# Kernel tuning notes

Measured on AMD Instinct MI355X. Metric: run time of the kernel, lower is better.

Reference implementation:

```python
import jax, jax.numpy as jnp
import numpy as np

G = 128          # resolution
NE = 4           # n_emotions
SIGMA = 0.05     # splat kernel width
ETA = 0.01       # global write strength
ALPHA_H = 0.002
ALPHA_E = 0.001
LEAK = 5e-05
RADIUS = max(2, int(3.0 * SIGMA * G / 2.0))   # = 9
W = 2 * RADIUS + 1                            # = 19


def _laplacian(x):
    # 6-neighbor Laplacian with replicate padding; x: [..., G, G, G]
    pad = [(0, 0)] * (x.ndim - 3) + [(1, 1)] * 3
    p = jnp.pad(x, pad, mode='edge')
    c = p[..., 1:-1, 1:-1, 1:-1]
    return (p[..., :-2, 1:-1, 1:-1] + p[..., 2:, 1:-1, 1:-1]
            + p[..., 1:-1, :-2, 1:-1] + p[..., 1:-1, 2:, 1:-1]
            + p[..., 1:-1, 1:-1, :-2] + p[..., 1:-1, 1:-1, 2:]
            - 6.0 * c)


def _splat(H, E, positions, intensities, emotions):
    # Gaussian splat scatter-add into H [G,G,G] and E [NE,G,G,G].
    gp = (positions + 1.0) * 0.5 * (G - 1)                       # [N,3] grid coords
    c = jnp.clip(jnp.floor(gp).astype(jnp.int32), 0, G - 1)      # center cell
    offs = jnp.arange(-RADIUS, RADIUS + 1, dtype=jnp.int32)
    coords = c[:, :, None] + offs[None, None, :]                 # [N,3,W]
    valid = (coords >= 0) & (coords < G)
    cc = jnp.clip(coords, 0, G - 1)
    sig = SIGMA * G / 2.0
    d = coords.astype(gp.dtype) - gp[:, :, None]                 # [N,3,W]
    k1 = jnp.where(valid, jnp.exp(-(d * d) / (2.0 * sig * sig)), 0.0)
    kx, ky, kz = k1[:, 0], k1[:, 1], k1[:, 2]                    # [N,W] each (separable)
    omega = intensities * ETA                                    # [N]
    vals = (omega[:, None, None, None] * kx[:, :, None, None]
            * ky[:, None, :, None] * kz[:, None, None, :])       # [N,W,W,W]
    flat = ((cc[:, 0][:, :, None, None] * G + cc[:, 1][:, None, :, None]) * G
            + cc[:, 2][:, None, None, :]).reshape(-1)            # [N*W^3]
    H_new = H.reshape(-1).at[flat].add(vals.reshape(-1)).reshape(G, G, G)
    E_ch = []
    for e in range(NE):
        ve = (vals * emotions[:, e][:, None, None, None]).reshape(-1)
        E_ch.append(E[e].reshape(-1).at[flat].add(ve).reshape(G, G, G))
    return H_new, jnp.stack(E_ch)


def _step(H, E):
    H2 = jnp.maximum(H * (1.0 - LEAK) + ALPHA_H * _laplacian(H), 0.0)
    E2 = jnp.maximum(E * (1.0 - LEAK) + LEAK + ALPHA_E * _laplacian(E), 0.0)
    return H2, E2


def _sample(H, E, sp):
    # grid_sample trilinear, padding_mode='border', align_corners=True.
    # grid_sample axis convention: sp[...,0]->last axis, sp[...,1]->middle, sp[...,2]->first.
    B, T, _ = sp.shape
    t = jnp.clip((sp.reshape(-1, 3) + 1.0) * 0.5 * (G - 1), 0.0, G - 1)  # [BT,3]
    i0 = jnp.floor(t).astype(jnp.int32)
    f = t - i0
    i0 = jnp.clip(i0, 0, G - 1)
    i1 = jnp.clip(i0 + 1, 0, G - 1)
    x0, y0, z0 = i0[:, 0], i0[:, 1], i0[:, 2]
    x1, y1, z1 = i1[:, 0], i1[:, 1], i1[:, 2]
    fx, fy, fz = f[:, 0], f[:, 1], f[:, 2]

    def interp(vol):  # vol [..., G,G,G] -> [..., BT]
        out = 0.0
        for zi, wz in ((z0, 1.0 - fz), (z1, fz)):
            for yi, wy in ((y0, 1.0 - fy), (y1, fy)):
                for xi, wx in ((x0, 1.0 - fx), (x1, fx)):
                    out = out + vol[..., zi, yi, xi] * (wz * wy * wx)
        return out

    p_H = interp(H).reshape(B, T)
    p_E = interp(E).T.reshape(B, T, NE)
    return p_H, p_E


def setup_inputs() -> dict:
    key = jax.random.key(0)
    k1, k2, k3, k4 = jax.random.split(key, 4)
    N, B, T = 4096, 8, 1024
    return {
        'positions': jax.random.uniform(k1, (N, 3), jnp.float32, -0.95, 0.95),
        'intensities': jax.random.uniform(k2, (N,), jnp.float32),
        'emotions': jax.random.uniform(k3, (N, NE), jnp.float32),
        'sample_positions': jax.random.uniform(k4, (B, T, 3), jnp.float32, -1.0, 1.0),
        'H0': jnp.zeros((G, G, G), jnp.float32),
        'E0': jnp.ones((NE, G, G, G), jnp.float32),
    }


def reference(positions, intensities, emotions, sample_positions, H0, E0):
    H, E = _splat(H0, E0, positions, intensities, emotions)
    H, E = _step(H, E)
    p_H, p_E = _sample(H, E, sample_positions)
    return jnp.concatenate([p_H[..., None], p_E], axis=-1)  # [B,T,1+NE]
```

## Files before the change

### kernel.cpp

```cpp
#include <hip/hip_runtime.h>


namespace {
constexpr int   G      = 128;
constexpr int   G3     = G * G * G;
constexpr int   NE     = 4;
constexpr int   RAD    = 9;
constexpr float SIG    = 0.05f * (float)G * 0.5f;
constexpr float INV2S2 = 1.0f / (2.0f * SIG * SIG);
constexpr float ETA    = 0.01f;
constexpr float A_H    = 0.002f;
constexpr float A_E    = 0.001f;
constexpr float LEAK   = 5e-5f;

constexpr int T0 = 4, T1 = 4, T2 = 32;
constexpr int NT0 = G / T0, NT1 = G / T1, NT2 = G / T2;
constexpr int NTILES = NT0 * NT1 * NT2;
constexpr int CAP = 96;
}

__device__ __forceinline__ int clampi(int v, int lo, int hi) {
    return min(max(v, lo), hi);
}

__global__ void __launch_bounds__(256) bin_meta_kernel(
        const float* __restrict__ pos, const float* __restrict__ inten,
        const float4* __restrict__ emo4,
        int* __restrict__ counts, int* __restrict__ lists,
        float4* __restrict__ meta, int N) {
    const int p    = blockIdx.x * 4 + (threadIdx.x >> 6);
    const int lane = threadIdx.x & 63;
    if (p >= N) return;

    const float gx = (pos[p * 3 + 0] + 1.0f) * 0.5f * (float)(G - 1);
    const float gy = (pos[p * 3 + 1] + 1.0f) * 0.5f * (float)(G - 1);
    const float gz = (pos[p * 3 + 2] + 1.0f) * 0.5f * (float)(G - 1);
    const int c0 = clampi((int)floorf(gx), 0, G - 1);
    const int c1 = clampi((int)floorf(gy), 0, G - 1);
    const int c2 = clampi((int)floorf(gz), 0, G - 1);

    if (lane == 0) {
        meta[2 * p]     = make_float4(gx, gy, gz, inten[p] * ETA);
        meta[2 * p + 1] = emo4[p];
    }

    const int l0 = max(c0 - RAD, 0) >> 2, h0 = min(c0 + RAD, G - 1) >> 2;
    const int l1 = max(c1 - RAD, 0) >> 2, h1 = min(c1 + RAD, G - 1) >> 2;
    const int l2 = max(c2 - RAD, 0) >> 5, h2 = min(c2 + RAD, G - 1) >> 5;
    const int n0 = h0 - l0, n1 = h1 - l1, n2 = h2 - l2;

    for (int s = lane; s < 72; s += 64) {
        const int a = s / 12;
        const int r = s - a * 12;
        const int b = r >> 1;
        const int cs = r & 1;
        if (a <= n0 && b <= n1 && cs <= n2) {
            const int t = ((l0 + a) * NT1 + (l1 + b)) * NT2 + (l2 + cs);
            const int slot = atomicAdd(&counts[t], 1);
            if (slot < CAP) lists[t * CAP + slot] = p;
        }
    }
}

__global__ void __launch_bounds__(256) gather_kernel(
        const float4* __restrict__ meta,
        const float* __restrict__ H0, const float* __restrict__ E0,
        const int* __restrict__ counts, const int* __restrict__ lists,
        float* __restrict__ ws) {
    const int tile = blockIdx.x;
    const int t2 = tile % NT2, t1 = (tile / NT2) % NT1, t0 = tile / (NT2 * NT1);
    const int tid = threadIdx.x;

    __shared__ float kx[CAP * 4];
    __shared__ float ky[CAP * 4];
    __shared__ float kz[CAP * 32];

    const int cnt = min(counts[tile], CAP);
    const int* __restrict__ lst = lists + tile * CAP;

    const int b0 = t0 * T0, b1 = t1 * T1, b2 = t2 * T2;
    for (int t = tid; t < cnt * 40; t += 256) {
        const int n = t / 40;
        const int s = t - n * 40;
        const int p = lst[n];
        const int axis = (s < 4) ? 0 : (s < 8) ? 1 : 2;
        const int off  = (s < 4) ? s : (s < 8) ? s - 4 : s - 8;
        const float4 mg = meta[2 * p];
        const float g = (axis == 0) ? mg.x : (axis == 1) ? mg.y : mg.z;
        const int base = (axis == 0) ? b0 : (axis == 1) ? b1 : b2;
        const int cc = clampi((int)floorf(g), 0, G - 1);
        const int coord = base + off;
        const float d = (float)coord - g;
        float v = (abs(coord - cc) <= RAD) ? __expf(-d * d * INV2S2) : 0.0f;
        if (axis == 0) v *= mg.w;
        if (axis == 0)      kx[n * 4 + off] = v;
        else if (axis == 1) ky[n * 4 + off] = v;
        else                kz[n * 32 + off] = v;
    }
    __syncthreads();

    const int k  = tid & (T2 - 1);
    const int j  = (tid >> 5) & (T1 - 1);
    const int iA = tid >> 7;

    const int x2 = b2 + k, x1 = b1 + j, xA = b0 + iA, xB = xA + 2;
    const int flatA = (xA * G + x1) * G + x2;
    const int flatB = (xB * G + x1) * G + x2;

    float hA = H0[flatA], hB = H0[flatB];
    float eA[NE], eB[NE];
#pragma unroll
    for (int c = 0; c < NE; ++c) {
        eA[c] = E0[c * G3 + flatA];
        eB[c] = E0[c * G3 + flatB];
    }

    for (int n = 0; n < cnt; ++n) {
        const int p = lst[n];
        const float4 mm = meta[2 * p + 1];
        const float kyz = ky[n * 4 + j] * kz[n * 32 + k];
        const float kxA = kx[n * 4 + iA];
        const float kxB = kx[n * 4 + iA + 2];
        const float wA = kxA * kyz;
        const float wB = kxB * kyz;
        hA += wA;            hB += wB;
        eA[0] += wA * mm.x;  eB[0] += wB * mm.x;
        eA[1] += wA * mm.y;  eB[1] += wB * mm.y;
        eA[2] += wA * mm.z;  eB[2] += wB * mm.z;
        eA[3] += wA * mm.w;  eB[3] += wB * mm.w;
    }

    ws[flatA] = hA;  ws[flatB] = hB;
#pragma unroll
    for (int c = 0; c < NE; ++c) {
        ws[(c + 1) * G3 + flatA] = eA[c];
        ws[(c + 1) * G3 + flatB] = eB[c];
    }
}

__device__ __forceinline__ float stepped_at(const float* __restrict__ vol,
                                            int z, int y, int x,
                                            float addc, float alpha) {
    const int zm = max(z - 1, 0), zp = min(z + 1, G - 1);
    const int ym = max(y - 1, 0), yp = min(y + 1, G - 1);
    const int xm = max(x - 1, 0), xp = min(x + 1, G - 1);
    const float cv  = vol[(z * G + y) * G + x];
    const float lap = vol[(zm * G + y) * G + x] + vol[(zp * G + y) * G + x]
                    + vol[(z * G + ym) * G + x] + vol[(z * G + yp) * G + x]
                    + vol[(z * G + y) * G + xm] + vol[(z * G + y) * G + xp]
                    - 6.0f * cv;
    const float s = cv * (1.0f - LEAK) + addc + alpha * lap;
    return fmaxf(s, 0.0f);
}

__global__ void __launch_bounds__(256) sample_kernel(
        const float* __restrict__ sp, const float* __restrict__ ws,
        float* __restrict__ out, int n_out) {
    const int gt = blockIdx.x * blockDim.x + threadIdx.x;
    const int corner = gt & 7;
    const int o = gt >> 3;
    if (o >= n_out) return;
    const int c = o % 5;
    const int p = o / 5;

    const float t0 = fminf(fmaxf((sp[p * 3 + 0] + 1.0f) * 0.5f * (float)(G - 1), 0.0f), (float)(G - 1));
    const float t1 = fminf(fmaxf((sp[p * 3 + 1] + 1.0f) * 0.5f * (float)(G - 1), 0.0f), (float)(G - 1));
    const float t2 = fminf(fmaxf((sp[p * 3 + 2] + 1.0f) * 0.5f * (float)(G - 1), 0.0f), (float)(G - 1));

    const int a0 = (int)floorf(t0);  const float f0 = t0 - (float)a0;
    const int a1 = (int)floorf(t1);  const float f1 = t1 - (float)a1;
    const int a2 = (int)floorf(t2);  const float f2 = t2 - (float)a2;
    const int b0 = min(a0 + 1, G - 1);
    const int b1 = min(a1 + 1, G - 1);
    const int b2 = min(a2 + 1, G - 1);

    const int d0 = corner & 1, d1 = (corner >> 1) & 1, d2 = corner >> 2;
    const int   x = d0 ? b0 : a0;
    const int   y = d1 ? b1 : a1;
    const int   z = d2 ? b2 : a2;
    const float w = (d0 ? f0 : 1.0f - f0) * (d1 ? f1 : 1.0f - f1)
                  * (d2 ? f2 : 1.0f - f2);

    const float* vol  = ws + (size_t)c * G3;
    const float addc  = (c == 0) ? 0.0f : LEAK;
    const float alpha = (c == 0) ? A_H : A_E;

    float v = w * stepped_at(vol, z, y, x, addc, alpha);
    v += __shfl_xor(v, 1);
    v += __shfl_xor(v, 2);
    v += __shfl_xor(v, 4);
    if (corner == 0) out[o] = v;
}

extern "C" void kernel_launch(void* const* d_in, const int* in_sizes, int n_in,
                              void* d_out, int out_size, void* d_ws, size_t ws_size,
                              hipStream_t stream) {
    const float* positions   = (const float*)d_in[0];
    const float* intensities = (const float*)d_in[1];
    const float* emotions    = (const float*)d_in[2];
    const float* sample_pos  = (const float*)d_in[3];
    const float* H0          = (const float*)d_in[4];
    const float* E0          = (const float*)d_in[5];
    float* ws  = (float*)d_ws;
    float* out = (float*)d_out;

    const int N = in_sizes[0] / 3;

    int*    counts = (int*)(ws + 5 * (size_t)G3);
    int*    lists  = counts + NTILES;
    float4* meta   = (float4*)(lists + (size_t)NTILES * CAP);

    hipMemsetAsync(counts, 0, NTILES * sizeof(int), stream);

    bin_meta_kernel<<<(N + 3) / 4, 256, 0, stream>>>(
        positions, intensities, (const float4*)emotions, counts, lists, meta, N);

    gather_kernel<<<NTILES, 256, 0, stream>>>(
        meta, H0, E0, counts, lists, ws);

    const int n_thr = out_size * 8;
    sample_kernel<<<(n_thr + 255) / 256, 256, 0, stream>>>(
        sample_pos, ws, out, out_size);
}
```

Before: 134.9 us.

## Enlarge gather tiles to 4x8x32 with per-thread 4-voxel accumulation

Doubles the tile's y extent so each block covers 1024 voxels. Each thread now accumulates four x-voxels, reading the packed kx and emotion weights as float4 from shared memory instead of chasing the particle index and meta per iteration. This is meant to cut per-tile particle-list overhead and redundant global loads, at the cost of more registers per thread and a larger per-tile list capacity (raised to 128). The memset is also replaced by a small zeroing kernel.

```diff
diff --git a/kernel.cpp b/kernel.cpp
--- a/kernel.cpp
+++ b/kernel.cpp
@@ -13,14 +13,18 @@
 constexpr float A_E    = 0.001f;
 constexpr float LEAK   = 5e-5f;
 
-constexpr int T0 = 4, T1 = 4, T2 = 32;
+constexpr int T0 = 4, T1 = 8, T2 = 32;
 constexpr int NT0 = G / T0, NT1 = G / T1, NT2 = G / T2;
 constexpr int NTILES = NT0 * NT1 * NT2;
-constexpr int CAP = 96;
+constexpr int CAP = 128;
 }
 
 __device__ __forceinline__ int clampi(int v, int lo, int hi) {
     return min(max(v, lo), hi);
+}
+
+__global__ void zero_counts(int4* __restrict__ counts4) {
+    counts4[threadIdx.x + blockIdx.x * blockDim.x] = make_int4(0, 0, 0, 0);
 }
 
 __global__ void __launch_bounds__(256) bin_meta_kernel(
@@ -45,14 +49,14 @@
     }
 
     const int l0 = max(c0 - RAD, 0) >> 2, h0 = min(c0 + RAD, G - 1) >> 2;
-    const int l1 = max(c1 - RAD, 0) >> 2, h1 = min(c1 + RAD, G - 1) >> 2;
+    const int l1 = max(c1 - RAD, 0) >> 3, h1 = min(c1 + RAD, G - 1) >> 3;
     const int l2 = max(c2 - RAD, 0) >> 5, h2 = min(c2 + RAD, G - 1) >> 5;
     const int n0 = h0 - l0, n1 = h1 - l1, n2 = h2 - l2;
 
-    for (int s = lane; s < 72; s += 64) {
-        const int a = s / 12;
-        const int r = s - a * 12;
-        const int b = r >> 1;
+    if (lane < 48) {
+        const int a  = lane >> 3;
+        const int r  = lane & 7;
+        const int b  = r >> 1;
         const int cs = r & 1;
         if (a <= n0 && b <= n1 && cs <= n2) {
             const int t = ((l0 + a) * NT1 + (l1 + b)) * NT2 + (l2 + cs);
@@ -68,73 +72,83 @@
         const int* __restrict__ counts, const int* __restrict__ lists,
         float* __restrict__ ws) {
     const int tile = blockIdx.x;
-    const int t2 = tile % NT2, t1 = (tile / NT2) % NT1, t0 = tile / (NT2 * NT1);
+    const int t2 = tile & 3, t1 = (tile >> 2) & 15, t0 = tile >> 6;
     const int tid = threadIdx.x;
 
-    __shared__ float kx[CAP * 4];
-    __shared__ float ky[CAP * 4];
+    __shared__ __align__(16) float kxf[CAP * 4];
+    __shared__ __align__(16) float emf[CAP * 4];
+    __shared__ float ky[CAP * 8];
     __shared__ float kz[CAP * 32];
 
     const int cnt = min(counts[tile], CAP);
     const int* __restrict__ lst = lists + tile * CAP;
 
     const int b0 = t0 * T0, b1 = t1 * T1, b2 = t2 * T2;
-    for (int t = tid; t < cnt * 40; t += 256) {
-        const int n = t / 40;
-        const int s = t - n * 40;
+
+    for (int t = tid; t < cnt * 48; t += 256) {
+        const int n = t / 48;
+        const int s = t - n * 48;
         const int p = lst[n];
-        const int axis = (s < 4) ? 0 : (s < 8) ? 1 : 2;
-        const int off  = (s < 4) ? s : (s < 8) ? s - 4 : s - 8;
-        const float4 mg = meta[2 * p];
-        const float g = (axis == 0) ? mg.x : (axis == 1) ? mg.y : mg.z;
-        const int base = (axis == 0) ? b0 : (axis == 1) ? b1 : b2;
-        const int cc = clampi((int)floorf(g), 0, G - 1);
-        const int coord = base + off;
-        const float d = (float)coord - g;
-        float v = (abs(coord - cc) <= RAD) ? __expf(-d * d * INV2S2) : 0.0f;
-        if (axis == 0) v *= mg.w;
-        if (axis == 0)      kx[n * 4 + off] = v;
-        else if (axis == 1) ky[n * 4 + off] = v;
-        else                kz[n * 32 + off] = v;
+        if (s < 44) {
+            const float4 mg = meta[2 * p];
+            const int axis = (s >= 4) + (s >= 12);
+            const int off  = s - ((axis == 0) ? 0 : (axis == 1) ? 4 : 12);
+            const float g  = (axis == 0) ? mg.x : (axis == 1) ? mg.y : mg.z;
+            const int base = (axis == 0) ? b0 : (axis == 1) ? b1 : b2;
+            const int cc    = clampi((int)floorf(g), 0, G - 1);
+            const int coord = base + off;
+            const float d = (float)coord - g;
+            float v = (abs(coord - cc) <= RAD) ? __expf(-d * d * INV2S2) : 0.0f;
+            if (axis == 0) {
+                kxf[n * 4 + off] = v * mg.w;
+            } else if (axis == 1) {
+                ky[n * 8 + off] = v;
+            } else {
+                kz[n * 32 + off] = v;
+            }
+        } else {
+            const float4 me = meta[2 * p + 1];
+            const int q = s - 44;
+            emf[n * 4 + q] = (q == 0) ? me.x : (q == 1) ? me.y : (q == 2) ? me.z : me.w;
+        }
     }
     __syncthreads();
 
-    const int k  = tid & (T2 - 1);
-    const int j  = (tid >> 5) & (T1 - 1);
-    const int iA = tid >> 7;
-
-    const int x2 = b2 + k, x1 = b1 + j, xA = b0 + iA, xB = xA + 2;
-    const int flatA = (xA * G + x1) * G + x2;
-    const int flatB = (xB * G + x1) * G + x2;
-
-    float hA = H0[flatA], hB = H0[flatB];
-    float eA[NE], eB[NE];
-#pragma unroll
-    for (int c = 0; c < NE; ++c) {
-        eA[c] = E0[c * G3 + flatA];
-        eB[c] = E0[c * G3 + flatB];
-    }
+    const int k = tid & 31;
+    const int j = tid >> 5;
+    const int x2 = b2 + k, x1 = b1 + j;
+    const int flat0 = (b0 * G + x1) * G + x2;
+
+    float h[4], e[NE][4];
+#pragma unroll
+    for (int i = 0; i < 4; ++i) {
+        h[i] = H0[flat0 + i * G * G];
+#pragma unroll
+        for (int c = 0; c < NE; ++c) e[c][i] = E0[c * G3 + flat0 + i * G * G];
+    }
+
+    const float4* __restrict__ kx4 = (const float4*)kxf;
+    const float4* __restrict__ em4 = (const float4*)emf;
 
     for (int n = 0; n < cnt; ++n) {
-        const int p = lst[n];
-        const float4 mm = meta[2 * p + 1];
-        const float kyz = ky[n * 4 + j] * kz[n * 32 + k];
-        const float kxA = kx[n * 4 + iA];
-        const float kxB = kx[n * 4 + iA + 2];
-        const float wA = kxA * kyz;
-        const float wB = kxB * kyz;
-        hA += wA;            hB += wB;
-        eA[0] += wA * mm.x;  eB[0] += wB * mm.x;
-        eA[1] += wA * mm.y;  eB[1] += wB * mm.y;
-        eA[2] += wA * mm.z;  eB[2] += wB * mm.z;
-        eA[3] += wA * mm.w;  eB[3] += wB * mm.w;
-    }
-
-    ws[flatA] = hA;  ws[flatB] = hB;
-#pragma unroll
-    for (int c = 0; c < NE; ++c) {
-        ws[(c + 1) * G3 + flatA] = eA[c];
-        ws[(c + 1) * G3 + flatB] = eB[c];
+        const float4 kxv = kx4[n];
+        const float4 emv = em4[n];
+        const float kyz = ky[n * 8 + j] * kz[n * 32 + k];
+        const float w0 = kxv.x * kyz, w1 = kxv.y * kyz;
+        const float w2 = kxv.z * kyz, w3 = kxv.w * kyz;
+        h[0] += w0;  h[1] += w1;  h[2] += w2;  h[3] += w3;
+        e[0][0] += w0 * emv.x; e[0][1] += w1 * emv.x; e[0][2] += w2 * emv.x; e[0][3] += w3 * emv.x;
+        e[1][0] += w0 * emv.y; e[1][1] += w1 * emv.y; e[1][2] += w2 * emv.y; e[1][3] += w3 * emv.y;
+        e[2][0] += w0 * emv.z; e[2][1] += w1 * emv.z; e[2][2] += w2 * emv.z; e[2][3] += w3 * emv.z;
+        e[3][0] += w0 * emv.w; e[3][1] += w1 * emv.w; e[3][2] += w2 * emv.w; e[3][3] += w3 * emv.w;
+    }
+
+#pragma unroll
+    for (int i = 0; i < 4; ++i) {
+        ws[flat0 + i * G * G] = h[i];
+#pragma unroll
+        for (int c = 0; c < NE; ++c)
+            ws[(c + 1) * G3 + flat0 + i * G * G] = e[c][i];
     }
 }
 
@@ -210,7 +224,7 @@
     int*    lists  = counts + NTILES;
     float4* meta   = (float4*)(lists + (size_t)NTILES * CAP);
 
-    hipMemsetAsync(counts, 0, NTILES * sizeof(int), stream);
+    zero_counts<<<2, 256, 0, stream>>>((int4*)counts);
 
     bin_meta_kernel<<<(N + 3) / 4, 256, 0, stream>>>(
         positions, intensities, (const float4*)emotions, counts, lists, meta, N);
```

New measurement: 138.4 us. +2.6%, slower.
